# Performance work log

Hardware: AMD Instinct MI355X
Metric: run time of the kernel (lower is better)

Reference implementation:

```python
import jax, jax.numpy as jnp
import numpy as np

N_NODES = 50000
N_EDGES = 800000
F_IN = 128
F_OUT = 64
K = 8


def setup_inputs() -> dict:
    key = jax.random.key(0)
    k1, k2, k3, k4 = jax.random.split(key, 4)
    x = jax.random.normal(k1, (N_NODES, F_IN), dtype=jnp.float32)
    edge_index = jax.random.randint(k2, (2, N_EDGES), 0, N_NODES, dtype=jnp.int64)
    # ChebConv params: K per-order linear weights [F_in, F_out] + shared bias
    W = jax.random.normal(k3, (K, F_IN, F_OUT), dtype=jnp.float32) * 0.05
    b = jax.random.normal(k4, (F_OUT,), dtype=jnp.float32) * 0.05
    return {"x": x, "edge_index": edge_index, "W": W, "b": b}


def reference(x, edge_index, W, b):
    # ChebConv (PyG), norm='sym', lambda_max=2:
    #   L_hat = 2L/lambda_max - I  ->  diag = 0, off-diag = -d_src^{-1/2} d_dst^{-1/2}
    # T_0 = x, T_1 = L_hat x, T_k = 2 L_hat T_{k-1} - T_{k-2}
    # out = sum_k T_k @ W_k + b, then ReLU (from KipfNet_simple.forward)
    N = x.shape[0]
    src, dst = edge_index[0], edge_index[1]
    ones = jnp.ones(src.shape[0], dtype=x.dtype)
    deg = jax.ops.segment_sum(ones, src, num_segments=N)  # scatter at row
    dis = jnp.where(deg > 0, jax.lax.rsqrt(jnp.maximum(deg, 1e-12)), 0.0)
    w = -dis[src] * dis[dst]  # [E] edge weights of L_hat (zero diagonal)

    def prop(t):
        # SpMM: aggregate messages w * t[src] at dst
        return jax.ops.segment_sum(w[:, None] * t[src], dst, num_segments=N)

    T_prev = x                       # T_0
    T_cur = prop(x)                  # T_1
    out = T_prev @ W[0] + T_cur @ W[1]
    for k in range(2, W.shape[0]):
        T_next = 2.0 * prop(T_cur) - T_prev
        out = out + T_next @ W[k]
        T_prev, T_cur = T_cur, T_next
    return jax.nn.relu(out + b)
```

## Files before the change

kernel.cpp:

```cpp
#include <hip/hip_runtime.h>

#define F_IN 128
#define F_OUT 64
#define CAP 64
#define PSZ 6400
#define BCH 64

typedef unsigned short ushort_t;
typedef unsigned char uchar_t;
typedef unsigned int uint_t;
typedef __attribute__((ext_vector_type(8))) short bf16x8;
typedef __attribute__((ext_vector_type(4))) float f32x4;

__device__ inline float bf2f(ushort_t h) {
    return __uint_as_float(((uint_t)h) << 16);
}
__device__ inline ushort_t f2b(float f) {
    uint_t u = __float_as_uint(f);
    return (ushort_t)((u + 0x7FFFu + ((u >> 16) & 1u)) >> 16);
}
__device__ inline int wscan_incl(int v, int lane) {
#pragma unroll
    for (int d = 1; d < 64; d <<= 1) {
        int u = __shfl_up(v, d);
        if (lane >= d) v += u;
    }
    return v;
}

__global__ __launch_bounds__(256) void count_kernel(
        const int* __restrict__ ei, int E, int N, int psz, int chunk,
        uchar_t* __restrict__ cmat, uchar_t* __restrict__ dmat) {
    __shared__ int lcnt[PSZ];
    __shared__ int ldeg[PSZ];
    int p = blockIdx.x >> 6, b = blockIdx.x & 63;
    int lo = p * psz;
    int hi = lo + psz; if (hi > N) hi = N;
    int span = hi - lo;
    int t = threadIdx.x;
    for (int i = t; i < span; i += 256) { lcnt[i] = 0; ldeg[i] = 0; }
    __syncthreads();
    int e0 = b * chunk, e1 = e0 + chunk; if (e1 > E) e1 = E;
    for (int e = e0 + t; e < e1; e += 256) {
        int s = ei[e], d = ei[E + e];
        unsigned sl = (unsigned)(s - lo), dl = (unsigned)(d - lo);
        if (sl < (unsigned)span) atomicAdd(&ldeg[sl], 1);
        if (dl < (unsigned)span) atomicAdd(&lcnt[dl], 1);
    }
    __syncthreads();
    for (int i = t; i < span; i += 256) {
        cmat[(size_t)b * N + lo + i] = (uchar_t)lcnt[i];
        dmat[(size_t)b * N + lo + i] = (uchar_t)ldeg[i];
    }
}

__global__ __launch_bounds__(256) void colscan_kernel(
        uchar_t* __restrict__ cmat, const uchar_t* __restrict__ dmat,
        int* __restrict__ total, float* __restrict__ dis,
        int* __restrict__ bsum, int N) {
    __shared__ int ws4[4];
    int t = threadIdx.x, lane = t & 63, w = t >> 6;
    int i = blockIdx.x * 256 + t;
    int run = 0;
    if (i < N) {
#pragma unroll 4
        for (int b = 0; b < BCH; ++b) {
            int v = cmat[(size_t)b * N + i];
            cmat[(size_t)b * N + i] = (uchar_t)run;
            run += v;
        }
        total[i] = run;
        int dg = 0;
#pragma unroll 4
        for (int b = 0; b < BCH; ++b) dg += dmat[(size_t)b * N + i];
        dis[i] = (dg > 0) ? rsqrtf((float)dg) : 0.0f;
    }
    int v = run;
#pragma unroll
    for (int d = 32; d >= 1; d >>= 1) v += __shfl_down(v, d);
    if (lane == 0) ws4[w] = v;
    __syncthreads();
    if (t == 0) bsum[blockIdx.x] = ws4[0] + ws4[1] + ws4[2] + ws4[3];
}

__global__ void bscan_kernel(const int* __restrict__ bsum, int* __restrict__ boff,
                             int G, int* __restrict__ rowptr, int N) {
    __shared__ int wsum[4]; __shared__ int wexcl[4];
    int t = threadIdx.x, lane = t & 63, w = t >> 6;
    int v = (t < G) ? bsum[t] : 0;
    int s = wscan_incl(v, lane);
    if (lane == 63) wsum[w] = s;
    __syncthreads();
    if (t == 0) {
        int a = 0;
#pragma unroll
        for (int j = 0; j < 4; ++j) { int tmp = wsum[j]; wexcl[j] = a; a += tmp; }
        rowptr[N] = a;
    }
    __syncthreads();
    if (t < G) boff[t] = wexcl[w] + s - v;
}

__global__ void rowptr_kernel(const int* __restrict__ cnt, const int* __restrict__ boff,
                              int* __restrict__ rowptr, int N) {
    __shared__ int wsum[4]; __shared__ int wexcl[4];
    int t = threadIdx.x, lane = t & 63, w = t >> 6;
    int i = blockIdx.x * 256 + t;
    int v = (i < N) ? cnt[i] : 0;
    int s = wscan_incl(v, lane);
    if (lane == 63) wsum[w] = s;
    __syncthreads();
    if (t == 0) {
        int a = 0;
#pragma unroll
        for (int j = 0; j < 4; ++j) { int tmp = wsum[j]; wexcl[j] = a; a += tmp; }
    }
    __syncthreads();
    if (i < N) rowptr[i] = boff[blockIdx.x] + wexcl[w] + s - v;
}

__global__ __launch_bounds__(256) void place_kernel(
        const int* __restrict__ ei, int E, int N, int psz, int chunk,
        const uchar_t* __restrict__ cmat, const int* __restrict__ rowptr,
        const float* __restrict__ dis, long long* __restrict__ csr8) {
    __shared__ int lbase[PSZ];
    int p = blockIdx.x >> 6, b = blockIdx.x & 63;
    int lo = p * psz;
    int hi = lo + psz; if (hi > N) hi = N;
    int span = hi - lo;
    int t = threadIdx.x;
    for (int i = t; i < span; i += 256)
        lbase[i] = rowptr[lo + i] + (int)cmat[(size_t)b * N + lo + i];
    __syncthreads();
    int e0 = b * chunk, e1 = e0 + chunk; if (e1 > E) e1 = E;
    for (int e = e0 + t; e < e1; e += 256) {
        int d = ei[E + e];
        unsigned dl = (unsigned)(d - lo);
        if (dl < (unsigned)span) {
            int s = ei[e];
            int slot = atomicAdd(&lbase[dl], 1);
            long long rec = ((long long)(unsigned)__float_as_uint(dis[s]) << 32) | (unsigned)s;
            __builtin_nontemporal_store(rec, &csr8[slot]);
        }
    }
}

__global__ void convert_kernel(const float* __restrict__ x, ushort_t* __restrict__ xb,
                               const float* __restrict__ W, ushort_t* __restrict__ Wt,
                               int xwork) {
    int idx = blockIdx.x * 256 + threadIdx.x;
    if (idx < xwork) {
        int base = idx * 8;
        float4 a = *(const float4*)(x + base);
        float4 b = *(const float4*)(x + base + 4);
        ushort_t h[8];
        h[0] = f2b(a.x); h[1] = f2b(a.y); h[2] = f2b(a.z); h[3] = f2b(a.w);
        h[4] = f2b(b.x); h[5] = f2b(b.y); h[6] = f2b(b.z); h[7] = f2b(b.w);
        *(uint4*)(xb + base) = *(const uint4*)h;
    } else {
        int widx = idx - xwork;
        if (widx >= 65536) return;
        int k = widx >> 13, rem = widx & 8191;
        int o = rem >> 7, f = rem & 127;
        Wt[widx] = f2b(W[k * 8192 + f * 64 + o]);
    }
}

#define WLS_STRIDE 136
__global__ __launch_bounds__(256) void ygemm_kernel(
        const ushort_t* __restrict__ xb, const ushort_t* __restrict__ Wt,
        ushort_t* __restrict__ Y, size_t planeE, int N) {
    __shared__ ushort_t Wls[64 * WLS_STRIDE];
    int t = threadIdx.x;
    int lane = t & 63, w = t >> 6;
    int quad = lane >> 4, col = lane & 15;
    int n0 = blockIdx.x * 64;

    int row = n0 + w * 16 + col;
    bool rowOK = row < N;

    uint4 aU[4];
#pragma unroll
    for (int fs = 0; fs < 4; ++fs) {
        aU[fs] = make_uint4(0, 0, 0, 0);
        if (rowOK) aU[fs] = *(const uint4*)(xb + (size_t)row * F_IN + fs * 32 + quad * 8);
    }

    for (int k = 0; k < 8; ++k) {
        const ushort_t* Wg = Wt + (size_t)k * 64 * 128;
        __syncthreads();
#pragma unroll
        for (int i = 0; i < 4; ++i) {
            int c16 = t + 256 * i;
            int o = c16 >> 4, ch = c16 & 15;
            uint4 v = *(const uint4*)(Wg + o * 128 + ch * 8);
            *(uint4*)(&Wls[o * WLS_STRIDE + ch * 8]) = v;
        }
        __syncthreads();

        f32x4 acc[4];
#pragma unroll
        for (int c = 0; c < 4; ++c) acc[c] = (f32x4){0.f, 0.f, 0.f, 0.f};
#pragma unroll
        for (int fs = 0; fs < 4; ++fs) {
            union { uint4 u; bf16x8 v; } a;
            a.u = aU[fs];
#pragma unroll
            for (int c = 0; c < 4; ++c) {
                union { uint4 u; bf16x8 v; } b;
                b.u = *(const uint4*)(&Wls[(c * 16 + col) * WLS_STRIDE + fs * 32 + quad * 8]);
                acc[c] = __builtin_amdgcn_mfma_f32_16x16x32_bf16(a.v, b.v, acc[c], 0, 0, 0);
            }
        }
        ushort_t* Yk = Y + (size_t)k * planeE;
#pragma unroll
        for (int c = 0; c < 4; ++c) {
#pragma unroll
            for (int r = 0; r < 4; ++r) {
                int node = n0 + w * 16 + quad * 4 + r;
                if (node >= N) continue;
                Yk[(size_t)node * F_OUT + c * 16 + col] = f2b(acc[c][r]);
            }
        }
    }
}

__global__ __launch_bounds__(256) void prop64_kernel(
        const ushort_t* __restrict__ bin, const ushort_t* __restrict__ addA,
        const ushort_t* addB, void* __restrict__ outp,
        const long long* __restrict__ csr8, const int* __restrict__ rowptr,
        const float* __restrict__ dis, const float* __restrict__ bias,
        int N, float scale, int mode) {
    int wave = threadIdx.x >> 6;
    int lane = threadIdx.x & 63;
    int node = blockIdx.x * 4 + wave;
    if (node >= N) return;
    int e0 = rowptr[node];
    int len = rowptr[node + 1] - e0;
    if (len > CAP) len = CAP;

    long long rec = 0;
    if (lane < len) rec = csr8[e0 + lane];
    int sIdx = (int)(unsigned)(rec & 0xFFFFFFFFll);
    float wL = __uint_as_float((uint_t)((unsigned long long)rec >> 32));

    int g = lane >> 3;
    int f8 = lane & 7;

    uint4 bb[4];
    float wv[4];
#pragma unroll
    for (int it = 0; it < 4; ++it) {
        int jj = it * 8 + g;
        int s = __shfl(sIdx, jj);
        float w = __shfl(wL, jj);
        bool ok = jj < len;
        wv[it] = ok ? w : 0.f;
        s = ok ? s : 0;
        bb[it] = *(const uint4*)(bin + (size_t)s * F_OUT + f8 * 8);
    }

    float acc[8];
#pragma unroll
    for (int i = 0; i < 8; ++i) acc[i] = 0.f;
#pragma unroll
    for (int it = 0; it < 4; ++it) {
        const ushort_t* h = (const ushort_t*)&bb[it];
#pragma unroll
        for (int i = 0; i < 8; ++i) acc[i] += wv[it] * bf2f(h[i]);
    }

    for (int j0 = 32; j0 < len; j0 += 8) {
        int jj = j0 + g;
        int s = __shfl(sIdx, jj);
        float w = __shfl(wL, jj);
        bool ok = jj < len;
        w = ok ? w : 0.f;
        s = ok ? s : 0;
        uint4 raw = *(const uint4*)(bin + (size_t)s * F_OUT + f8 * 8);
        const ushort_t* h = (const ushort_t*)&raw;
#pragma unroll
        for (int i = 0; i < 8; ++i) acc[i] += w * bf2f(h[i]);
    }

#pragma unroll
    for (int i = 0; i < 8; ++i) {
        acc[i] += __shfl_xor(acc[i], 8);
        acc[i] += __shfl_xor(acc[i], 16);
        acc[i] += __shfl_xor(acc[i], 32);
    }

    if (lane < 8) {
        float m = -dis[node] * scale;
        float r[8];
#pragma unroll
        for (int i = 0; i < 8; ++i) r[i] = m * acc[i];
        {
            uint4 raw = *(const uint4*)(addA + (size_t)node * F_OUT + lane * 8);
            const ushort_t* h = (const ushort_t*)&raw;
#pragma unroll
            for (int i = 0; i < 8; ++i) r[i] += bf2f(h[i]);
        }
        if (addB) {
            uint4 raw = *(const uint4*)(addB + (size_t)node * F_OUT + lane * 8);
            const ushort_t* h = (const ushort_t*)&raw;
#pragma unroll
            for (int i = 0; i < 8; ++i) r[i] -= bf2f(h[i]);
        }
        if (mode == 0) {
            ushort_t o[8];
#pragma unroll
            for (int i = 0; i < 8; ++i) o[i] = f2b(r[i]);
            *(uint4*)((ushort_t*)outp + (size_t)node * F_OUT + lane * 8) = *(const uint4*)o;
        } else {
            float* po = (float*)outp + (size_t)node * F_OUT + lane * 8;
            float vv[8];
#pragma unroll
            for (int i = 0; i < 8; ++i) {
                float v = r[i] + bias[lane * 8 + i];
                vv[i] = v > 0.f ? v : 0.f;
            }
            *(float4*)po = make_float4(vv[0], vv[1], vv[2], vv[3]);
            *(float4*)(po + 4) = make_float4(vv[4], vv[5], vv[6], vv[7]);
        }
    }
}

extern "C" void kernel_launch(void* const* d_in, const int* in_sizes, int n_in,
                              void* d_out, int out_size, void* d_ws, size_t ws_size,
                              hipStream_t stream) {
    const float* x  = (const float*)d_in[0];
    const int*   ei = (const int*)d_in[1];
    const float* W  = (const float*)d_in[2];
    const float* b  = (const float*)d_in[3];
    float* out = (float*)d_out;

    int N = in_sizes[0] / F_IN;
    int E = in_sizes[1] / 2;

    char* ws = (char*)d_ws;
    size_t off = 0;
    auto alloc = [&](size_t bytes) -> void* {
        void* p = ws + off;
        off = (off + bytes + 255) & ~(size_t)255;
        return p;
    };
    int G = (N + 255) / 256;
    int psz = (N + 7) / 8;
    int chunk = (E + BCH - 1) / BCH;
    size_t planeE = (size_t)N * F_OUT;

    int*       total = (int*)alloc((size_t)N * 4);
    int*       rowptr= (int*)alloc((size_t)(N + 1) * 4);
    int*       bsum  = (int*)alloc((size_t)G * 4);
    int*       boff  = (int*)alloc((size_t)G * 4);
    float*     dis   = (float*)alloc((size_t)N * 4);
    long long* csr8  = (long long*)alloc((size_t)(E + 64) * 8);
    ushort_t*  Wt    = (ushort_t*)alloc((size_t)8 * 64 * 128 * 2);
    uchar_t*   cmat  = (uchar_t*)alloc((size_t)BCH * N);
    uchar_t*   dmat  = (uchar_t*)alloc((size_t)BCH * N);
    ushort_t*  xb    = (ushort_t*)alloc((size_t)N * F_IN * 2);
    ushort_t*  Y     = (ushort_t*)alloc(8 * planeE * 2 + 16384);
    ushort_t*  B[7];
    for (int k = 1; k < 7; ++k) B[k] = (ushort_t*)alloc(planeE * 2 + 16384);
    ushort_t* b7 = Y + 7 * planeE;

    count_kernel<<<8 * BCH, 256, 0, stream>>>(ei, E, N, psz, chunk, cmat, dmat);
    colscan_kernel<<<G, 256, 0, stream>>>(cmat, dmat, total, dis, bsum, N);
    bscan_kernel<<<1, 256, 0, stream>>>(bsum, boff, G, rowptr, N);
    rowptr_kernel<<<G, 256, 0, stream>>>(total, boff, rowptr, N);
    place_kernel<<<8 * BCH, 256, 0, stream>>>(ei, E, N, psz, chunk, cmat, rowptr, dis, csr8);

    int xwork = N * 16;
    convert_kernel<<<(xwork + 65536 + 255) / 256, 256, 0, stream>>>(x, xb, W, Wt, xwork);

    int gemm_blocks = (N + 63) / 64;
    ygemm_kernel<<<gemm_blocks, 256, 0, stream>>>(xb, Wt, Y, planeE, N);

    int prop_blocks = (N + 3) / 4;
    const ushort_t* bk1 = b7;
    const ushort_t* bk2 = nullptr;
    for (int k = 6; k >= 1; --k) {
        ushort_t* bk = B[k];
        prop64_kernel<<<prop_blocks, 256, 0, stream>>>(
            bk1, Y + (size_t)k * planeE, bk2, bk, csr8, rowptr, dis, b, N, 2.0f, 0);
        bk2 = bk1; bk1 = bk;
    }
    prop64_kernel<<<prop_blocks, 256, 0, stream>>>(
        bk1 , Y , bk2 , out, csr8, rowptr, dis, b, N, 1.0f, 1);
}
```

Baseline: 335.6 us.

## Pack histogram counters into bytes and fuse block scan into rowptr kernel

The count kernel now keeps its per-node counters as packed 8-bit fields inside 32-bit shared words, so each block can cover four partitions instead of eight. This halves the number of edge-scanning blocks in the count and place kernels, and so halves the redundant reads of the edge list. The separate single-block scan over block sums is removed: each rowptr block reduces the preceding block sums itself. The risks are that a byte counter overflows if one chunk puts more than 255 edges on a node, that fewer blocks reduce parallelism, and that place_kernel now needs about 50KB of shared memory, which may lower occupancy.

```diff
diff --git a/kernel.cpp b/kernel.cpp
--- a/kernel.cpp
+++ b/kernel.cpp
@@ -3,7 +3,7 @@
 #define F_IN 128
 #define F_OUT 64
 #define CAP 64
-#define PSZ 6400
+#define PSZ4 12544
 #define BCH 64
 
 typedef unsigned short ushort_t;
@@ -31,26 +31,27 @@
 __global__ __launch_bounds__(256) void count_kernel(
         const int* __restrict__ ei, int E, int N, int psz, int chunk,
         uchar_t* __restrict__ cmat, uchar_t* __restrict__ dmat) {
-    __shared__ int lcnt[PSZ];
-    __shared__ int ldeg[PSZ];
+    __shared__ uint_t lcnt4[PSZ4 / 4];
+    __shared__ uint_t ldeg4[PSZ4 / 4];
     int p = blockIdx.x >> 6, b = blockIdx.x & 63;
     int lo = p * psz;
     int hi = lo + psz; if (hi > N) hi = N;
     int span = hi - lo;
     int t = threadIdx.x;
-    for (int i = t; i < span; i += 256) { lcnt[i] = 0; ldeg[i] = 0; }
+    int nwords = (span + 3) >> 2;
+    for (int i = t; i < nwords; i += 256) { lcnt4[i] = 0; ldeg4[i] = 0; }
     __syncthreads();
     int e0 = b * chunk, e1 = e0 + chunk; if (e1 > E) e1 = E;
     for (int e = e0 + t; e < e1; e += 256) {
         int s = ei[e], d = ei[E + e];
         unsigned sl = (unsigned)(s - lo), dl = (unsigned)(d - lo);
-        if (sl < (unsigned)span) atomicAdd(&ldeg[sl], 1);
-        if (dl < (unsigned)span) atomicAdd(&lcnt[dl], 1);
+        if (sl < (unsigned)span) atomicAdd(&ldeg4[sl >> 2], 1u << ((sl & 3) * 8));
+        if (dl < (unsigned)span) atomicAdd(&lcnt4[dl >> 2], 1u << ((dl & 3) * 8));
     }
     __syncthreads();
     for (int i = t; i < span; i += 256) {
-        cmat[(size_t)b * N + lo + i] = (uchar_t)lcnt[i];
-        dmat[(size_t)b * N + lo + i] = (uchar_t)ldeg[i];
+        cmat[(size_t)b * N + lo + i] = (uchar_t)((lcnt4[i >> 2] >> ((i & 3) * 8)) & 0xFF);
+        dmat[(size_t)b * N + lo + i] = (uchar_t)((ldeg4[i >> 2] >> ((i & 3) * 8)) & 0xFF);
     }
 }
 
@@ -83,11 +84,24 @@
     if (t == 0) bsum[blockIdx.x] = ws4[0] + ws4[1] + ws4[2] + ws4[3];
 }
 
-__global__ void bscan_kernel(const int* __restrict__ bsum, int* __restrict__ boff,
-                             int G, int* __restrict__ rowptr, int N) {
+__global__ __launch_bounds__(256) void rowptr_kernel(
+        const int* __restrict__ total, const int* __restrict__ bsum,
+        int* __restrict__ rowptr, int N, int G) {
+    __shared__ int ws4[4];
     __shared__ int wsum[4]; __shared__ int wexcl[4];
+    __shared__ int sboff;
     int t = threadIdx.x, lane = t & 63, w = t >> 6;
-    int v = (t < G) ? bsum[t] : 0;
+    int blk = blockIdx.x;
+    int part = (t < blk && t < G) ? bsum[t] : 0;
+    int pv = part;
+#pragma unroll
+    for (int d = 32; d >= 1; d >>= 1) pv += __shfl_down(pv, d);
+    if (lane == 0) ws4[w] = pv;
+    __syncthreads();
+    if (t == 0) sboff = ws4[0] + ws4[1] + ws4[2] + ws4[3];
+    __syncthreads();
+    int i = blk * 256 + t;
+    int v = (i < N) ? total[i] : 0;
     int s = wscan_incl(v, lane);
     if (lane == 63) wsum[w] = s;
     __syncthreads();
@@ -95,35 +109,20 @@
         int a = 0;
 #pragma unroll
         for (int j = 0; j < 4; ++j) { int tmp = wsum[j]; wexcl[j] = a; a += tmp; }
-        rowptr[N] = a;
-    }
-    __syncthreads();
-    if (t < G) boff[t] = wexcl[w] + s - v;
-}
-
-__global__ void rowptr_kernel(const int* __restrict__ cnt, const int* __restrict__ boff,
-                              int* __restrict__ rowptr, int N) {
-    __shared__ int wsum[4]; __shared__ int wexcl[4];
-    int t = threadIdx.x, lane = t & 63, w = t >> 6;
-    int i = blockIdx.x * 256 + t;
-    int v = (i < N) ? cnt[i] : 0;
-    int s = wscan_incl(v, lane);
-    if (lane == 63) wsum[w] = s;
-    __syncthreads();
-    if (t == 0) {
-        int a = 0;
-#pragma unroll
-        for (int j = 0; j < 4; ++j) { int tmp = wsum[j]; wexcl[j] = a; a += tmp; }
-    }
-    __syncthreads();
-    if (i < N) rowptr[i] = boff[blockIdx.x] + wexcl[w] + s - v;
+    }
+    __syncthreads();
+    if (i < N) {
+        int excl = sboff + wexcl[w] + s - v;
+        rowptr[i] = excl;
+        if (i == N - 1) rowptr[N] = excl + v;
+    }
 }
 
 __global__ __launch_bounds__(256) void place_kernel(
         const int* __restrict__ ei, int E, int N, int psz, int chunk,
         const uchar_t* __restrict__ cmat, const int* __restrict__ rowptr,
         const float* __restrict__ dis, long long* __restrict__ csr8) {
-    __shared__ int lbase[PSZ];
+    __shared__ int lbase[PSZ4];
     int p = blockIdx.x >> 6, b = blockIdx.x & 63;
     int lo = p * psz;
     int hi = lo + psz; if (hi > N) hi = N;
@@ -346,14 +345,13 @@
         return p;
     };
     int G = (N + 255) / 256;
-    int psz = (N + 7) / 8;
+    int psz = (N + 3) / 4;
     int chunk = (E + BCH - 1) / BCH;
     size_t planeE = (size_t)N * F_OUT;
 
     int*       total = (int*)alloc((size_t)N * 4);
     int*       rowptr= (int*)alloc((size_t)(N + 1) * 4);
     int*       bsum  = (int*)alloc((size_t)G * 4);
-    int*       boff  = (int*)alloc((size_t)G * 4);
     float*     dis   = (float*)alloc((size_t)N * 4);
     long long* csr8  = (long long*)alloc((size_t)(E + 64) * 8);
     ushort_t*  Wt    = (ushort_t*)alloc((size_t)8 * 64 * 128 * 2);
@@ -365,11 +363,10 @@
     for (int k = 1; k < 7; ++k) B[k] = (ushort_t*)alloc(planeE * 2 + 16384);
     ushort_t* b7 = Y + 7 * planeE;
 
-    count_kernel<<<8 * BCH, 256, 0, stream>>>(ei, E, N, psz, chunk, cmat, dmat);
+    count_kernel<<<4 * BCH, 256, 0, stream>>>(ei, E, N, psz, chunk, cmat, dmat);
     colscan_kernel<<<G, 256, 0, stream>>>(cmat, dmat, total, dis, bsum, N);
-    bscan_kernel<<<1, 256, 0, stream>>>(bsum, boff, G, rowptr, N);
-    rowptr_kernel<<<G, 256, 0, stream>>>(total, boff, rowptr, N);
-    place_kernel<<<8 * BCH, 256, 0, stream>>>(ei, E, N, psz, chunk, cmat, rowptr, dis, csr8);
+    rowptr_kernel<<<G, 256, 0, stream>>>(total, bsum, rowptr, N, G);
+    place_kernel<<<4 * BCH, 256, 0, stream>>>(ei, E, N, psz, chunk, cmat, rowptr, dis, csr8);
 
     int xwork = N * 16;
     convert_kernel<<<(xwork + 65536 + 255) / 256, 256, 0, stream>>>(x, xb, W, Wt, xwork);
```

Measured after the change: 334.1 us. Within noise of the previous version (-0.5%).
